# Optimization experiments

Measured on AMD Instinct MI355X. Metric: run time of the kernel, lower is better.

Reference implementation:

```python
import jax, jax.numpy as jnp
import numpy as np

K_BINS, EMB_WIDTH = 2048, 64
N, T = 8, 8192

def setup_inputs() -> dict:
    key = jax.random.key(0)
    k1, k2 = jax.random.split(key)
    x = jax.random.normal(k1, (N, EMB_WIDTH, T), dtype=jnp.float32)
    mask = jnp.ones((N, 1, T), dtype=jnp.float32)
    k = jax.random.normal(k2, (K_BINS, EMB_WIDTH), dtype=jnp.float32)
    return {"x": x, "mask": mask, "k": k}

def reference(x, mask, k):
    # Faithful forward of BottleneckBlock.forward with update_k=False and
    # codebook `k` already initialized (init path is a stateful randperm init).
    n, c, t = x.shape
    w = k.shape[1]
    # preprocess: [N, W, T] -> [N*T, W]
    xf = jnp.transpose(x, (0, 2, 1)).reshape(-1, c)
    mf = jnp.transpose(mask, (0, 2, 1)).reshape(-1, 1)
    prenorm = jnp.linalg.norm(xf - jnp.mean(xf)) / np.sqrt(float(xf.size))
    dist = (jnp.sum(xf * xf, axis=-1, keepdims=True)
            - 2.0 * (xf @ k.T)
            + jnp.sum(k * k, axis=-1)[None, :])  # [N*T, k_bins]
    x_l = jnp.argmin(dist, axis=-1)              # [N*T]
    fit = jax.lax.stop_gradient(jnp.mean(jnp.min(dist, axis=-1)))
    x_d = jax.lax.stop_gradient(k[x_l])          # dequantize, no_grad in torch
    # commit loss: mask is 0/1, so masked-row norm^2 == sum(mask * diff^2)
    diff2 = jnp.sum((x_d - xf) ** 2, axis=-1, keepdims=True)
    commit_loss = jnp.sum(mf * diff2) / (jnp.sum(mf) * w)
    # straight-through estimator + mask
    x_d = (xf + jax.lax.stop_gradient(x_d - xf)) * mf
    # postprocess: back to [N, W, T] and [N, T]
    x_d = jnp.transpose(x_d.reshape(n, t, w), (0, 2, 1))
    x_l = x_l.reshape(n, t)
    return x_l, x_d, commit_loss, fit, prenorm
```

## Files before the change

### kernel.cpp

```cpp
#include <hip/hip_runtime.h>

#define T_DIM 8192
#define N_DIM 8
#define C_DIM 64
#define KB    2048
#define NT    (N_DIM * T_DIM)
#define TOTX  ((size_t)NT * C_DIM)
#define NBLK  2048
#define LISTCAP 65536
#define TAU   0.045f

#define SCR_COUNT 0
#define SCR_LIST  16
#define SCR_PART  65792
#define SCR_KK    82432
#define SCR_K     90112
#define SCR_FIX   262144
#define WS_NEED_BYTES ((size_t)1310720 * 4)

typedef _Float16 half_t;
typedef _Float16 f16x8 __attribute__((ext_vector_type(8)));
typedef float    f32x16 __attribute__((ext_vector_type(16)));

__device__ __forceinline__ float np_sumsq64(const float* __restrict__ a) {
    float r[8];
    #pragma unroll
    for (int j = 0; j < 8; ++j) r[j] = __fmul_rn(a[j], a[j]);
    #pragma unroll
    for (int i = 8; i < 64; i += 8)
        #pragma unroll
        for (int j = 0; j < 8; ++j)
            r[j] = __fadd_rn(r[j], __fmul_rn(a[i + j], a[i + j]));
    return __fadd_rn(__fadd_rn(__fadd_rn(r[0], r[1]), __fadd_rn(r[2], r[3])),
                     __fadd_rn(__fadd_rn(r[4], r[5]), __fadd_rn(r[6], r[7])));
}

__global__ __launch_bounds__(64) void kprep_kernel(const float* __restrict__ k,
                                                   float* __restrict__ base) {
    const int bin = blockIdx.x * 64 + threadIdx.x;
    if (bin == 0) ((int*)base)[SCR_COUNT] = 0;

    float kv[64];
    #pragma unroll
    for (int i = 0; i < 16; ++i)
        *(float4*)&kv[i * 4] = *(const float4*)(k + (size_t)bin * 64 + i * 4);

    float kn = 0.f;
    #pragma unroll
    for (int c = 0; c < 64; ++c) kn = fmaf(kv[c], kv[c], kn);
    base[SCR_KK + bin] = np_sumsq64(kv);

    f16x8* kscr = (f16x8*)(base + SCR_K);
    const int ch = bin >> 7, b127 = bin & 127;
    #pragma unroll
    for (int slot = 0; slot < 8; ++slot) {
        f16x8 h8;
        #pragma unroll
        for (int e = 0; e < 8; ++e)
            h8[e] = (half_t)(-2.f * (float)((half_t)kv[slot * 8 + e]));
        kscr[(size_t)ch * 1152 + slot * 128 + b127] = h8;
    }
    {
        half_t knh = (half_t)kn;
        half_t knl = (half_t)(kn - (float)knh);
        f16x8 k8;
        #pragma unroll
        for (int e = 0; e < 8; ++e) k8[e] = (half_t)0.f;
        k8[0] = knh; k8[1] = knl;
        kscr[(size_t)ch * 1152 + 1024 + b127] = k8;
    }
}

template <int WSMODE>
__global__ __launch_bounds__(256, 2) void argmin_kernel(const float* __restrict__ x,
                                                        const float* __restrict__ mask,
                                                        const float* __restrict__ k,
                                                        float* __restrict__ out,
                                                        float* __restrict__ base) {
    __shared__ __align__(16) f16x8 xhi_s[256];
    __shared__ float psx[8][32], psxx[8][32];
    __shared__ float wres[4][32][3];
    __shared__ int   sbest_s[32];

    const int tid = threadIdx.x;
    const int l   = tid & 63, w = tid >> 6;
    const int col = l & 31, kg = l >> 5;
    const int r0  = blockIdx.x * 32;
    const int n   = r0 >> 13;
    const int t0  = r0 & (T_DIM - 1);

    {
        const int row = tid & 31, slot = tid >> 5;
        float sx = 0.f, sxx = 0.f;
        f16x8 h8;
        #pragma unroll
        for (int e = 0; e < 8; ++e) {
            float v = x[((size_t)n * C_DIM + slot * 8 + e) * T_DIM + t0 + row];
            h8[e] = (half_t)v;
            sx += v; sxx = fmaf(v, v, sxx);
        }
        xhi_s[slot * 32 + row] = h8;
        psx[slot][row]  = sx;
        psxx[slot][row] = sxx;
    }
    __syncthreads();

    f16x8 a0 = xhi_s[(0 + kg) * 32 + col];
    f16x8 a1 = xhi_s[(2 + kg) * 32 + col];
    f16x8 a2 = xhi_s[(4 + kg) * 32 + col];
    f16x8 a3 = xhi_s[(6 + kg) * 32 + col];
    f16x8 aones;
    #pragma unroll
    for (int e = 0; e < 8; ++e) aones[e] = (half_t)0.f;
    if (kg == 0) { aones[0] = (half_t)1.f; aones[1] = (half_t)1.f; }

    const f16x8* kf0 = (const f16x8*)(base + SCR_K) + (size_t)w * 4 * 1152 + col;
    const int kgo = kg * 128;

    f32x16 zacc;
    #pragma unroll
    for (int r = 0; r < 16; ++r) zacc[r] = 0.f;

    float bv0 = __builtin_inff(), b20 = __builtin_inff();
    float bv1 = __builtin_inff(), b21 = __builtin_inff();
    float bv2 = __builtin_inff(), b22 = __builtin_inff();
    float bv3 = __builtin_inff(), b23 = __builtin_inff();

    f16x8 bA[4], bB[4], b4A, b4B;

#define LOADT(t, BH, B4)                                            \
    {                                                               \
        const f16x8* p = kf0 + (((t) >> 2) * 1152 + ((t) & 3) * 32);\
        BH[0] = p[kgo]; BH[1] = p[kgo + 256];                       \
        BH[2] = p[kgo + 512]; BH[3] = p[kgo + 768];                 \
        B4 = p[1024];                                               \
    }

#define UPD(J, RR, CODE)                                                     \
    {                                                                        \
        float spf = __uint_as_float(                                         \
            (__float_as_uint(acc[RR]) & 0xFFFFFFC0u) | (unsigned)(CODE));    \
        float nb2;                                                           \
        asm("v_med3_f32 %0, %1, %2, %3"                                      \
            : "=v"(nb2) : "v"(spf), "v"(bv##J), "v"(b2##J));                 \
        b2##J = nb2;                                                         \
        bv##J = fminf(bv##J, spf);                                           \
    }

#define COMPT(t, BH, B4)                                                     \
    {                                                                        \
        f32x16 acc = __builtin_amdgcn_mfma_f32_32x32x16_f16(B4, aones, zacc, 0, 0, 0); \
        acc = __builtin_amdgcn_mfma_f32_32x32x16_f16(BH[0], a0, acc, 0, 0, 0); \
        acc = __builtin_amdgcn_mfma_f32_32x32x16_f16(BH[1], a1, acc, 0, 0, 0); \
        acc = __builtin_amdgcn_mfma_f32_32x32x16_f16(BH[2], a2, acc, 0, 0, 0); \
        acc = __builtin_amdgcn_mfma_f32_32x32x16_f16(BH[3], a3, acc, 0, 0, 0); \
        const int cb4 = (t) * 4;                                             \
        UPD(0, 0, cb4 + 0)  UPD(0, 1, cb4 + 1)  UPD(0, 2, cb4 + 2)  UPD(0, 3, cb4 + 3) \
        UPD(1, 4, cb4 + 0)  UPD(1, 5, cb4 + 1)  UPD(1, 6, cb4 + 2)  UPD(1, 7, cb4 + 3) \
        UPD(2, 8, cb4 + 0)  UPD(2, 9, cb4 + 1)  UPD(2, 10, cb4 + 2) UPD(2, 11, cb4 + 3) \
        UPD(3, 12, cb4 + 0) UPD(3, 13, cb4 + 1) UPD(3, 14, cb4 + 2) UPD(3, 15, cb4 + 3) \
    }

    LOADT(0, bA, b4A);
    #pragma unroll 1
    for (int t = 0; t < 14; t += 2) {
        LOADT(t + 1, bB, b4B);
        COMPT(t, bA, b4A);
        LOADT(t + 2, bA, b4A);
        COMPT(t + 1, bB, b4B);
    }
    LOADT(15, bB, b4B);
    COMPT(14, bA, b4A);
    COMPT(15, bB, b4B);
#undef LOADT
#undef COMPT
#undef UPD

    const int bbase = w * 512 + 4 * kg;
    int c0, c1, c2, c3;
    {
        unsigned q;
        q = __float_as_uint(bv0) & 63u; c0 = bbase + (int)(q >> 2) * 32 + 0  + (int)(q & 3);
        q = __float_as_uint(bv1) & 63u; c1 = bbase + (int)(q >> 2) * 32 + 8  + (int)(q & 3);
        q = __float_as_uint(bv2) & 63u; c2 = bbase + (int)(q >> 2) * 32 + 16 + (int)(q & 3);
        q = __float_as_uint(bv3) & 63u; c3 = bbase + (int)(q >> 2) * 32 + 24 + (int)(q & 3);
    }

    float bv, b2; int bb;
    {
        float m01v; int m01c; float m01s;
        if (bv1 < bv0 || (bv1 == bv0 && c1 < c0)) { m01v = bv1; m01c = c1; }
        else                                      { m01v = bv0; m01c = c0; }
        m01s = fminf(fminf(b20, b21), fmaxf(bv0, bv1));
        float m23v; int m23c; float m23s;
        if (bv3 < bv2 || (bv3 == bv2 && c3 < c2)) { m23v = bv3; m23c = c3; }
        else                                      { m23v = bv2; m23c = c2; }
        m23s = fminf(fminf(b22, b23), fmaxf(bv2, bv3));
        if (m23v < m01v || (m23v == m01v && m23c < m01c)) { bv = m23v; bb = m23c; }
        else                                              { bv = m01v; bb = m01c; }
        b2 = fminf(fminf(m01s, m23s), fmaxf(m01v, m23v));
    }

    {
        float ov = __shfl_xor(bv, 32, 64);
        float o2 = __shfl_xor(b2, 32, 64);
        int   ob = __shfl_xor(bb, 32, 64);
        b2 = fminf(fminf(b2, o2), fmaxf(bv, ov));
        if (ov < bv || (ov == bv && ob < bb)) { bv = ov; bb = ob; }
    }

    if (kg == 0) {
        wres[w][col][0] = bv;
        wres[w][col][1] = b2;
        wres[w][col][2] = __int_as_float(bb);
    }
    __syncthreads();

    if (tid < 32) {
        const int row = tid;
        const float v0 = wres[0][row][0], v1 = wres[1][row][0];
        const float v2 = wres[2][row][0], v3 = wres[3][row][0];
        float fbv = v0; int fbb = __float_as_int(wres[0][row][2]);
        if (v1 < fbv) { fbv = v1; fbb = __float_as_int(wres[1][row][2]); }
        if (v2 < fbv) { fbv = v2; fbb = __float_as_int(wres[2][row][2]); }
        if (v3 < fbv) { fbv = v3; fbb = __float_as_int(wres[3][row][2]); }
        const float m01 = fminf(v0, v1), M01 = fmaxf(v0, v1);
        const float m23 = fminf(v2, v3), M23 = fmaxf(v2, v3);
        const float sec = fminf(fmaxf(m01, m23), fminf(M01, M23));
        const float fb2 = fminf(sec,
            fminf(fminf(wres[0][row][1], wres[1][row][1]),
                  fminf(wres[2][row][1], wres[3][row][1])));

        out[r0 + row] = (float)fbb;
        sbest_s[row] = fbb;
        if (fb2 - fbv < TAU) {
            int idx = atomicAdd((int*)base + SCR_COUNT, 1);
            if (idx < LISTCAP) ((int*)base + SCR_LIST)[idx] = r0 + row;
        }
        float sx = 0.f, sxx = 0.f;
        #pragma unroll
        for (int sp = 0; sp < 8; ++sp) { sx += psx[sp][row]; sxx += psxx[sp][row]; }
        const float m  = mask[r0 + row];
        const float d2 = sxx + fbv;
        float vals[5] = { m * d2, d2, m, sx, sxx };
        #pragma unroll
        for (int off = 1; off <= 16; off <<= 1)
            #pragma unroll
            for (int q = 0; q < 5; ++q) vals[q] += __shfl_xor(vals[q], off, 64);
        if (tid == 0) {
            float* partials = base + SCR_PART;
            #pragma unroll
            for (int q = 0; q < 5; ++q)
                partials[(size_t)blockIdx.x * 8 + q] = vals[q];
        }
    }

    if (WSMODE) {
        __syncthreads();
        const int row = tid & 31, slot = tid >> 5;
        const int b = sbest_s[row];
        const float m = mask[r0 + row];
        float* xd = out + NT;
        #pragma unroll
        for (int e = 0; e < 8; ++e)
            xd[((size_t)n * C_DIM + slot * 8 + e) * T_DIM + t0 + row] =
                k[(size_t)b * C_DIM + slot * 8 + e] * m;
    }
}

__global__ __launch_bounds__(256) void fixup_kernel(const float* __restrict__ x,
                                                    const float* __restrict__ k,
                                                    float* __restrict__ base) {
    __shared__ float xs[32][65];
    __shared__ float sxx_s[32];
    __shared__ float redv[256];
    __shared__ int   redb[256];

    const int tid = threadIdx.x;
    const int* count    = (const int*)base + SCR_COUNT;
    const int* flaglist = (const int*)base + SCR_LIST;
    const float* kk     = base + SCR_KK;
    float* fix          = base + SCR_FIX;
    int cnt = *count;
    if (cnt > LISTCAP) cnt = LISTCAP;
    const int nb8 = ((cnt + 31) >> 5) << 3;

    const int rloc = tid & 31, part = tid >> 5;

    for (int wk = blockIdx.x; wk < nb8; wk += gridDim.x) {
        const int bi = wk >> 3, chunk = wk & 7;
        int li = bi * 32 + rloc;
        if (li >= cnt) li = bi * 32;
        const int row = flaglist[li];
        const int n = row >> 13, t = row & (T_DIM - 1);
        #pragma unroll
        for (int e = 0; e < 8; ++e)
            xs[rloc][part * 8 + e] = x[((size_t)n * C_DIM + part * 8 + e) * T_DIM + t];
        __syncthreads();
        if (tid < 32) sxx_s[tid] = np_sumsq64(&xs[tid][0]);
        __syncthreads();

        float xr[64];
        #pragma unroll
        for (int c = 0; c < 64; ++c) xr[c] = xs[rloc][c];
        const float xx = sxx_s[rloc];

        float bv = __builtin_inff();
        int   bb = 0x7fffffff;
        const int bbase = chunk * 256 + part * 32;
        #pragma unroll 1
        for (int i = 0; i < 32; i += 2) {
            const int b0 = bbase + i;
            const int b1 = b0 + 1;
            const float* k0 = k + (size_t)b0 * 64;
            const float* k1 = k + (size_t)b1 * 64;
            float d0 = 0.f, d1 = 0.f;
            #pragma unroll
            for (int c = 0; c < 64; ++c) {
                d0 = fmaf(xr[c], k0[c], d0);
                d1 = fmaf(xr[c], k1[c], d1);
            }
            float s0 = __fadd_rn(__fsub_rn(xx, __fadd_rn(d0, d0)), kk[b0]);
            float s1 = __fadd_rn(__fsub_rn(xx, __fadd_rn(d1, d1)), kk[b1]);
            if (s0 < bv || (s0 == bv && b0 < bb)) { bv = s0; bb = b0; }
            if (s1 < bv || (s1 == bv && b1 < bb)) { bv = s1; bb = b1; }
        }
        redv[tid] = bv; redb[tid] = bb;
        __syncthreads();
        if (tid < 32) {
            float fv = redv[tid]; int fb = redb[tid];
            #pragma unroll
            for (int p = 1; p < 8; ++p) {
                float ov = redv[p * 32 + tid];
                int   ob = redb[p * 32 + tid];
                if (ov < fv || (ov == fv && ob < fb)) { fv = ov; fb = ob; }
            }
            const int fi = bi * 32 + tid;
            if (fi < cnt) {
                fix[(size_t)fi * 16 + chunk * 2]     = fv;
                fix[(size_t)fi * 16 + chunk * 2 + 1] = __int_as_float(fb);
            }
        }
        __syncthreads();
    }
}

template <int WSMODE>
__global__ __launch_bounds__(256) void fixmerge_kernel(const float* __restrict__ mask,
                                                       const float* __restrict__ k,
                                                       float* __restrict__ out,
                                                       float* __restrict__ base) {
    const int* count    = (const int*)base + SCR_COUNT;
    const int* flaglist = (const int*)base + SCR_LIST;
    const float* fix    = base + SCR_FIX;
    const int tid = threadIdx.x;
    int cnt = *count;
    if (cnt > LISTCAP) cnt = LISTCAP;

    for (int fi = blockIdx.x * 256 + tid; fi < cnt; fi += gridDim.x * 256) {
        const float* p = fix + (size_t)fi * 16;
        float bv = p[0];
        int   bb = __float_as_int(p[1]);
        #pragma unroll
        for (int c = 1; c < 8; ++c) {
            float v = p[c * 2];
            int   b = __float_as_int(p[c * 2 + 1]);
            if (v < bv || (v == bv && b < bb)) { bv = v; bb = b; }
        }
        const int row = flaglist[fi];
        out[row] = (float)bb;
        if (WSMODE) {
            const int n = row >> 13, t = row & (T_DIM - 1);
            const float m = mask[row];
            const float* kr = k + (size_t)bb * C_DIM;
            float* xd = out + NT;
            #pragma unroll
            for (int c = 0; c < C_DIM; ++c)
                xd[((size_t)n * C_DIM + c) * T_DIM + t] = kr[c] * m;
        }
    }

    if (blockIdx.x == 0) {
        const float* partials = base + SCR_PART;
        double vals[5] = {0, 0, 0, 0, 0};
        for (int i = tid; i < NBLK; i += 256)
            #pragma unroll
            for (int q = 0; q < 5; ++q) vals[q] += (double)partials[(size_t)i * 8 + q];
        #pragma unroll
        for (int off = 1; off <= 32; off <<= 1)
            #pragma unroll
            for (int q = 0; q < 5; ++q) vals[q] += __shfl_xor(vals[q], off, 64);
        __shared__ double sred[4][5];
        const int wid = tid >> 6, lane = tid & 63;
        if (lane == 0)
            for (int q = 0; q < 5; ++q) sred[wid][q] = vals[q];
        __syncthreads();
        if (tid == 0) {
            double cm  = sred[0][0] + sred[1][0] + sred[2][0] + sred[3][0];
            double fs  = sred[0][1] + sred[1][1] + sred[2][1] + sred[3][1];
            double ms  = sred[0][2] + sred[1][2] + sred[2][2] + sred[3][2];
            double sx  = sred[0][3] + sred[1][3] + sred[2][3] + sred[3][3];
            double sxx = sred[0][4] + sred[1][4] + sred[2][4] + sred[3][4];
            double sz  = (double)TOTX;
            out[NT + TOTX + 0] = (float)(cm / (ms * (double)C_DIM));
            out[NT + TOTX + 1] = (float)(fs / (double)NT);
            out[NT + TOTX + 2] = (float)sqrt(fmax(0.0, (sxx - sx * sx / sz) / sz));
        }
    }
}

__global__ __launch_bounds__(256) void xd_kernel(const float* __restrict__ mask,
                                                 const float* __restrict__ k,
                                                 float* __restrict__ out) {
    const int row = blockIdx.x * 256 + threadIdx.x;
    const int n = row >> 13, t = row & (T_DIM - 1);
    const int b = (int)out[row];
    const float m = mask[row];
    const float* kr = k + (size_t)b * C_DIM;
    float* xd = out + NT;
    #pragma unroll
    for (int c = 0; c < C_DIM; ++c)
        xd[((size_t)n * C_DIM + c) * T_DIM + t] = kr[c] * m;
}

extern "C" void kernel_launch(void* const* d_in, const int* in_sizes, int n_in,
                              void* d_out, int out_size, void* d_ws, size_t ws_size,
                              hipStream_t stream) {
    (void)in_sizes; (void)n_in; (void)out_size;
    const float* x    = (const float*)d_in[0];
    const float* mask = (const float*)d_in[1];
    const float* k    = (const float*)d_in[2];
    float* out = (float*)d_out;

    if (ws_size >= WS_NEED_BYTES) {
        float* base = (float*)d_ws;
        kprep_kernel<<<32, 64, 0, stream>>>(k, base);
        argmin_kernel<1><<<NBLK, 256, 0, stream>>>(x, mask, k, out, base);
        fixup_kernel<<<2048, 256, 0, stream>>>(x, k, base);
        fixmerge_kernel<1><<<256, 256, 0, stream>>>(mask, k, out, base);
    } else {
        float* base = out + NT;
        kprep_kernel<<<32, 64, 0, stream>>>(k, base);
        argmin_kernel<0><<<NBLK, 256, 0, stream>>>(x, mask, k, out, base);
        fixup_kernel<<<2048, 256, 0, stream>>>(x, k, base);
        fixmerge_kernel<0><<<256, 256, 0, stream>>>(mask, k, out, base);
        xd_kernel<<<NT / 256, 256, 0, stream>>>(mask, k, out);
    }
}
```

Measured before the change: 92.64 us.

## Deepen codebook prefetch to four buffers and move dequantized output to separate kernel

```diff
diff --git a/kernel.cpp b/kernel.cpp
--- a/kernel.cpp
+++ b/kernel.cpp
@@ -71,16 +71,13 @@
     }
 }
 
-template <int WSMODE>
 __global__ __launch_bounds__(256, 2) void argmin_kernel(const float* __restrict__ x,
                                                         const float* __restrict__ mask,
-                                                        const float* __restrict__ k,
                                                         float* __restrict__ out,
                                                         float* __restrict__ base) {
     __shared__ __align__(16) f16x8 xhi_s[256];
     __shared__ float psx[8][32], psxx[8][32];
     __shared__ float wres[4][32][3];
-    __shared__ int   sbest_s[32];
 
     const int tid = threadIdx.x;
     const int l   = tid & 63, w = tid >> 6;
@@ -126,7 +123,7 @@
     float bv2 = __builtin_inff(), b22 = __builtin_inff();
     float bv3 = __builtin_inff(), b23 = __builtin_inff();
 
-    f16x8 bA[4], bB[4], b4A, b4B;
+    f16x8 bA[4], bB[4], bC[4], bD[4], b4A, b4B, b4C, b4D;
 
 #define LOADT(t, BH, B4)                                            \
     {                                                               \
@@ -161,17 +158,18 @@
         UPD(3, 12, cb4 + 0) UPD(3, 13, cb4 + 1) UPD(3, 14, cb4 + 2) UPD(3, 15, cb4 + 3) \
     }
 
-    LOADT(0, bA, b4A);
+    LOADT(0, bA, b4A); LOADT(1, bB, b4B);
     #pragma unroll 1
-    for (int t = 0; t < 14; t += 2) {
-        LOADT(t + 1, bB, b4B);
-        COMPT(t, bA, b4A);
-        LOADT(t + 2, bA, b4A);
-        COMPT(t + 1, bB, b4B);
-    }
-    LOADT(15, bB, b4B);
-    COMPT(14, bA, b4A);
-    COMPT(15, bB, b4B);
+    for (int t = 0; t < 12; t += 4) {
+        LOADT(t + 2, bC, b4C); COMPT(t,     bA, b4A);
+        LOADT(t + 3, bD, b4D); COMPT(t + 1, bB, b4B);
+        LOADT(t + 4, bA, b4A); COMPT(t + 2, bC, b4C);
+        LOADT(t + 5, bB, b4B); COMPT(t + 3, bD, b4D);
+    }
+    LOADT(14, bC, b4C); COMPT(12, bA, b4A);
+    LOADT(15, bD, b4D); COMPT(13, bB, b4B);
+    COMPT(14, bC, b4C);
+    COMPT(15, bD, b4D);
 #undef LOADT
 #undef COMPT
 #undef UPD
@@ -232,7 +230,6 @@
                   fminf(wres[2][row][1], wres[3][row][1])));
 
         out[r0 + row] = (float)fbb;
-        sbest_s[row] = fbb;
         if (fb2 - fbv < TAU) {
             int idx = atomicAdd((int*)base + SCR_COUNT, 1);
             if (idx < LISTCAP) ((int*)base + SCR_LIST)[idx] = r0 + row;
@@ -253,18 +250,6 @@
             for (int q = 0; q < 5; ++q)
                 partials[(size_t)blockIdx.x * 8 + q] = vals[q];
         }
-    }
-
-    if (WSMODE) {
-        __syncthreads();
-        const int row = tid & 31, slot = tid >> 5;
-        const int b = sbest_s[row];
-        const float m = mask[r0 + row];
-        float* xd = out + NT;
-        #pragma unroll
-        for (int e = 0; e < 8; ++e)
-            xd[((size_t)n * C_DIM + slot * 8 + e) * T_DIM + t0 + row] =
-                k[(size_t)b * C_DIM + slot * 8 + e] * m;
     }
 }
 
@@ -345,10 +330,7 @@
     }
 }
 
-template <int WSMODE>
-__global__ __launch_bounds__(256) void fixmerge_kernel(const float* __restrict__ mask,
-                                                       const float* __restrict__ k,
-                                                       float* __restrict__ out,
+__global__ __launch_bounds__(256) void fixmerge_kernel(float* __restrict__ out,
                                                        float* __restrict__ base) {
     const int* count    = (const int*)base + SCR_COUNT;
     const int* flaglist = (const int*)base + SCR_LIST;
@@ -367,17 +349,7 @@
             int   b = __float_as_int(p[c * 2 + 1]);
             if (v < bv || (v == bv && b < bb)) { bv = v; bb = b; }
         }
-        const int row = flaglist[fi];
-        out[row] = (float)bb;
-        if (WSMODE) {
-            const int n = row >> 13, t = row & (T_DIM - 1);
-            const float m = mask[row];
-            const float* kr = k + (size_t)bb * C_DIM;
-            float* xd = out + NT;
-            #pragma unroll
-            for (int c = 0; c < C_DIM; ++c)
-                xd[((size_t)n * C_DIM + c) * T_DIM + t] = kr[c] * m;
-        }
+        out[flaglist[fi]] = (float)bb;
     }
 
     if (blockIdx.x == 0) {
@@ -431,19 +403,11 @@
     const float* mask = (const float*)d_in[1];
     const float* k    = (const float*)d_in[2];
     float* out = (float*)d_out;
-
-    if (ws_size >= WS_NEED_BYTES) {
-        float* base = (float*)d_ws;
-        kprep_kernel<<<32, 64, 0, stream>>>(k, base);
-        argmin_kernel<1><<<NBLK, 256, 0, stream>>>(x, mask, k, out, base);
-        fixup_kernel<<<2048, 256, 0, stream>>>(x, k, base);
-        fixmerge_kernel<1><<<256, 256, 0, stream>>>(mask, k, out, base);
-    } else {
-        float* base = out + NT;
-        kprep_kernel<<<32, 64, 0, stream>>>(k, base);
-        argmin_kernel<0><<<NBLK, 256, 0, stream>>>(x, mask, k, out, base);
-        fixup_kernel<<<2048, 256, 0, stream>>>(x, k, base);
-        fixmerge_kernel<0><<<256, 256, 0, stream>>>(mask, k, out, base);
-        xd_kernel<<<NT / 256, 256, 0, stream>>>(mask, k, out);
-    }
-}
+    float* base = (ws_size >= WS_NEED_BYTES) ? (float*)d_ws : out + NT;
+
+    kprep_kernel<<<32, 64, 0, stream>>>(k, base);
+    argmin_kernel<<<NBLK, 256, 0, stream>>>(x, mask, out, base);
+    fixup_kernel<<<2048, 256, 0, stream>>>(x, k, base);
+    fixmerge_kernel<<<256, 256, 0, stream>>>(out, base);
+    xd_kernel<<<NT / 256, 256, 0, stream>>>(mask, k, out);
+}
```

Result: faster. 84.09 us (-9.2%).
